# Performance work log

Hardware: AMD Instinct MI355X
Metric: run time of the kernel (lower is better)

Reference implementation:

```python
import jax, jax.numpy as jnp
import numpy as np

EPS = 1e-8

def _penalty(v, lo, hi):
    # if v<lo: (lo-v)/lo ; elif v>hi (hi finite): (v-hi)/hi ; else 0
    below = (lo - v) / lo
    if np.isinf(hi):
        return jnp.where(v < lo, below, 0.0)
    above = (v - hi) / hi
    return jnp.where(v < lo, below, jnp.where(v > hi, above, 0.0))

def _symbolic_features(x):
    # x: [B, input_dim]; column mapping from the original per-row loop
    am, bod, do, ph, nit = x[:, 0], x[:, 1], x[:, 2], x[:, 4], x[:, 7]
    # penalties in param_order = [ph, ammonia, bod, dissolved_oxygen, nitrate]
    p_ph  = _penalty(ph, 6.5, 8.5)
    p_am  = _penalty(am, 0.001, 0.5)
    p_bod = _penalty(bod, 0.001, 5.0)
    p_do  = _penalty(do, 6.0, np.inf)
    p_nit = _penalty(nit, 0.001, 10.0)
    # pollutant scores (missing params like 'nitrogen'/'orthophosphate' are skipped -> count adjusts)
    s_bact = (1.2 * am / (0.5 + EPS) + 1.5 * bod / (5.0 + EPS) - 0.8 * do / (10.0 + EPS)) / 3.0
    s_chem = (1.5 * ph / (8.5 + EPS) + 1.0 * nit / (10.0 + EPS)) / 2.0
    s_org  = (2.0 * bod / (5.0 + EPS) - 1.5 * do / (10.0 + EPS) + 0.8 * am / (0.5 + EPS)) / 3.0
    s_agr  = (2.0 * nit / (10.0 + EPS)) / 1.0
    resil = 1.0 / (1.0 + (p_ph + p_am + p_bod + p_do + p_nit) + EPS)
    return jnp.stack([p_ph, p_am, p_bod, p_do, p_nit, s_bact, s_chem, s_org, s_agr, resil], axis=1)

def setup_inputs() -> dict:
    key = jax.random.key(0)
    ks = jax.random.split(key, 16)
    B, D_IN, SYM, H = 1048576, 10, 10, 64
    def lin(k, fin, fout):
        k1, k2 = jax.random.split(k)
        s = 1.0 / np.sqrt(fin)
        return (jax.random.uniform(k1, (fin, fout), jnp.float32, -s, s),
                jax.random.uniform(k2, (fout,), jnp.float32, -s, s))
    W_sym, b_sym = lin(ks[0], SYM, H // 2)
    W_in, b_in = lin(ks[1], D_IN + H // 2, H)
    W1, b1 = lin(ks[2], H, H)
    W2, b2 = lin(ks[3], H, H)
    W3, b3 = lin(ks[4], H, H)
    W_r1, b_r1 = lin(ks[5], H, H // 2)
    W_r2, b_r2 = lin(ks[6], H // 2, 1)
    W_c1, b_c1 = lin(ks[7], H, H // 2)
    W_c2, b_c2 = lin(ks[8], H // 2, 4)
    x = jax.random.uniform(ks[9], (B, D_IN), jnp.float32)
    return {"x": x, "W_sym": W_sym, "b_sym": b_sym, "W_in": W_in, "b_in": b_in,
            "W1": W1, "b1": b1, "W2": W2, "b2": b2, "W3": W3, "b3": b3,
            "W_r1": W_r1, "b_r1": b_r1, "W_r2": W_r2, "b_r2": b_r2,
            "W_c1": W_c1, "b_c1": b_c1, "W_c2": W_c2, "b_c2": b_c2}

def reference(x, W_sym, b_sym, W_in, b_in, W1, b1, W2, b2, W3, b3,
              W_r1, b_r1, W_r2, b_r2, W_c1, b_c1, W_c2, b_c2):
    elu = jax.nn.elu
    sym = _symbolic_features(x)                      # [B, 10]
    sym_enc = elu(sym @ W_sym + b_sym)               # [B, 32]  (Dropout: eval mode = identity)
    h = elu(jnp.concatenate([x, sym_enc], axis=1) @ W_in + b_in)  # [B, 64]
    for W, b in ((W1, b1), (W2, b2), (W3, b3)):
        h = h + elu(h @ W + b)                       # residual MLP stack
    predictions = elu(h @ W_r1 + b_r1) @ W_r2 + b_r2            # [B, 1]
    pollutant_logits = elu(h @ W_c1 + b_c1) @ W_c2 + b_c2       # [B, 4]
    return predictions, pollutant_logits
```

## Files before the change

kernel.cpp:

```cpp
#include <hip/hip_runtime.h>
#include <hip/hip_bf16.h>
#include <math.h>

#define NROWS 1048576
#define EPSF 1e-8f

typedef unsigned short ushortT;
typedef __attribute__((ext_vector_type(8))) short short8;
typedef __attribute__((ext_vector_type(4))) float floatx4;
typedef __attribute__((ext_vector_type(4))) int intx4;

#define WS_HI   256
#define WS_LO   41216
#define WS_MF   82176
#define MF_B5   0
#define MF_WSYM 320
#define MF_BSYM 640
#define MF_WR2  672
#define MF_BR2  704
#define MF_WC2  708
#define MF_BC2  836
#define MF_WC2T 840

#define LDS_FENCE() asm volatile("s_waitcnt lgkmcnt(0)" ::: "memory")

struct WPtrs { const void* p[19]; };

__global__ void sniff_kernel(const ushortT* __restrict__ x, int* __restrict__ flag) {
    if (threadIdx.x == 0 && blockIdx.x == 0) {
        unsigned s = 0;
        for (int i = 0; i < 64; ++i) s |= (unsigned)(x[i] & 0x8000u);
        *flag = s ? 1 : 0;
    }
}

__device__ __forceinline__ float ldw(const void* p, int i, bool f32) {
    return f32 ? ((const float*)p)[i]
               : __uint_as_float(((unsigned)((const ushortT*)p)[i]) << 16);
}

__global__ void prep_kernel(WPtrs wp, const int* __restrict__ flag, void* __restrict__ ws) {
    const bool f32 = (*flag != 0);
    ushortT* hi = (ushortT*)((char*)ws + WS_HI);
    ushortT* lo = (ushortT*)((char*)ws + WS_LO);
    float* mf = (float*)((char*)ws + WS_MF);
    const int B = blockIdx.x;
    if (B < 5) {
        for (int idx = threadIdx.x; idx < 4096; idx += 256) {
            const int j = idx & 7, ln = (idx >> 3) & 63, t = (idx >> 9) & 3, s = idx >> 11;
            const int k = s * 32 + (ln >> 4) * 8 + j;
            const int n = t * 16 + (ln & 15);
            float w = 0.0f;
            if (B == 0)      { if (k < 42) w = ldw(wp.p[3], k * 64 + n, f32); }
            else if (B <= 3) { w = ldw(wp.p[3 + 2 * B], k * 64 + n, f32); }
            else             { w = (n < 32) ? ldw(wp.p[11], k * 32 + n, f32)
                                            : ldw(wp.p[15], k * 32 + (n - 32), f32); }
            const unsigned u = __float_as_uint(w);
            const float rem = w - __uint_as_float(u & 0xffff0000u);
            hi[B * 4096 + idx] = (ushortT)(u >> 16);
            lo[B * 4096 + idx] = (ushortT)(__float_as_uint(rem) >> 16);
        }
    } else {
        const int src[12] = {4, 6, 8, 10, 12, 16, 1, 2, 13, 14, 17, 18};
        const int cnt[12] = {64, 64, 64, 64, 32, 32, 320, 32, 32, 1, 128, 4};
        const int dst[12] = {0, 64, 128, 192, 256, 288, MF_WSYM, MF_BSYM, MF_WR2, MF_BR2, MF_WC2, MF_BC2};
        for (int a = 0; a < 12; ++a)
            for (int i = threadIdx.x; i < cnt[a]; i += 256)
                mf[dst[a] + i] = ldw(wp.p[src[a]], i, f32);
        for (int i = threadIdx.x; i < 128; i += 256) {
            const int qq = i >> 5, j = i & 31;
            mf[MF_WC2T + i] = ldw(wp.p[17], j * 4 + qq, f32);
        }
    }
}

__device__ __forceinline__ float eluf(float v) {
    return fmaxf(v, 0.0f) + (__expf(fminf(v, 0.0f)) - 1.0f);
}

__device__ __forceinline__ unsigned pack_hi16(unsigned ua, unsigned ub) {
    return __builtin_amdgcn_perm(ub, ua, 0x07060302u);
}

__device__ __forceinline__ void split8(const floatx4 f0, const floatx4 f1,
                                       short8& ahi, short8& alo) {
    float fv[8];
    #pragma unroll
    for (int i = 0; i < 4; ++i) { fv[i] = f0[i]; fv[4 + i] = f1[i]; }
    intx4 hi_i, lo_i;
    #pragma unroll
    for (int d = 0; d < 4; ++d) {
        const float a = fv[2 * d], b = fv[2 * d + 1];
        const unsigned ua = __float_as_uint(a), ub = __float_as_uint(b);
        hi_i[d] = (int)pack_hi16(ua, ub);
        const float la = a - __uint_as_float(ua & 0xffff0000u);
        const float lb = b - __uint_as_float(ub & 0xffff0000u);
        lo_i[d] = (int)pack_hi16(__float_as_uint(la), __float_as_uint(lb));
    }
    ahi = __builtin_bit_cast(short8, hi_i);
    alo = __builtin_bit_cast(short8, lo_i);
}

template<bool F32>
__device__ __forceinline__ void run_body(
    const void* __restrict__ xin, const char* __restrict__ wsb,
    void* __restrict__ out, float (* __restrict__ hb)[68],
    const int lane, const int rowg)
{
    const ushortT* __restrict__ wfhi = (const ushortT*)(wsb + WS_HI);
    const ushortT* __restrict__ wflo = (const ushortT*)(wsb + WS_LO);
    const float* __restrict__ mf = (const float*)(wsb + WS_MF);
    const int m = lane & 15, q = lane >> 4;

    #pragma unroll
    for (int it = 0; it < 6; ++it) {
        const int i = lane + (it << 6);
        if (i < 352) hb[i & 15][42 + (i >> 4)] = 0.0f;
    }

    float bias[5][4];
    #pragma unroll
    for (int L = 0; L < 5; ++L)
        #pragma unroll
        for (int t = 0; t < 4; ++t)
            bias[L][t] = mf[MF_B5 + L * 64 + t * 16 + m];

    float x[10];
    if (F32) {
        const float* xp = (const float*)xin + (size_t)rowg * 10;
        #pragma unroll
        for (int i = 0; i < 10; ++i) x[i] = xp[i];
    } else {
        const unsigned* xd = (const unsigned*)((const ushortT*)xin + (size_t)rowg * 10);
        #pragma unroll
        for (int i = 0; i < 5; ++i) {
            const unsigned d = xd[i];
            x[2 * i]     = __uint_as_float(d << 16);
            x[2 * i + 1] = __uint_as_float(d & 0xffff0000u);
        }
    }
    if (q == 0) {
        #pragma unroll
        for (int i = 0; i < 10; ++i) hb[m][i] = x[i];
    }

    const float am = x[0], bod = x[1], dox = x[2], ph = x[4], nit = x[7];
    const float p_ph  = ph  < 6.5f   ? (6.5f - ph) * 0.15384616f
                      : (ph > 8.5f   ? (ph - 8.5f) * 0.11764706f : 0.0f);
    const float p_am  = am  < 0.001f ? (0.001f - am) * 1000.0f
                      : (am > 0.5f   ? (am - 0.5f) * 2.0f : 0.0f);
    const float p_bod = bod < 0.001f ? (0.001f - bod) * 1000.0f
                      : (bod > 5.0f  ? (bod - 5.0f) * 0.2f : 0.0f);
    const float p_do  = dox < 6.0f   ? (6.0f - dox) * 0.16666667f : 0.0f;
    const float p_nit = nit < 0.001f ? (0.001f - nit) * 1000.0f
                      : (nit > 10.0f ? (nit - 10.0f) * 0.1f : 0.0f);
    const float s_bact = (am * 2.3999999f + bod * 0.29999998f - dox * 0.08f) * 0.33333334f;
    const float s_chem = (ph * 0.17647059f + nit * 0.1f) * 0.5f;
    const float s_org  = (bod * 0.39999998f - dox * 0.14999999f + am * 1.5999999f) * 0.33333334f;
    const float s_agr  = nit * 0.2f;
    const float resil  = 1.0f / (1.0f + (p_ph + p_am + p_bod + p_do + p_nit) + EPSF);
    const float sym[10] = {p_ph, p_am, p_bod, p_do, p_nit, s_bact, s_chem, s_org, s_agr, resil};

    float se[8];
    {
        const floatx4 b0 = *(const floatx4*)(mf + MF_BSYM + q * 8);
        const floatx4 b1 = *(const floatx4*)(mf + MF_BSYM + q * 8 + 4);
        #pragma unroll
        for (int jj = 0; jj < 4; ++jj) { se[jj] = b0[jj]; se[4 + jj] = b1[jj]; }
        #pragma unroll
        for (int k = 0; k < 10; ++k) {
            const floatx4 w0 = *(const floatx4*)(mf + MF_WSYM + k * 32 + q * 8);
            const floatx4 w1 = *(const floatx4*)(mf + MF_WSYM + k * 32 + q * 8 + 4);
            #pragma unroll
            for (int jj = 0; jj < 4; ++jj) {
                se[jj]     = fmaf(sym[k], w0[jj], se[jj]);
                se[4 + jj] = fmaf(sym[k], w1[jj], se[4 + jj]);
            }
        }
    }
    #pragma unroll
    for (int jj = 0; jj < 8; ++jj) hb[m][10 + q * 8 + jj] = eluf(se[jj]);
    LDS_FENCE();

    floatx4 hcd[4];
    #pragma unroll
    for (int L = 0; L < 5; ++L) {
        floatx4 acc[4];
        #pragma unroll
        for (int t = 0; t < 4; ++t) {
            const float b = bias[L][t];
            acc[t] = (floatx4){b, b, b, b};
        }
        #pragma unroll
        for (int s = 0; s < 2; ++s) {
            const floatx4 f0 = *(const floatx4*)&hb[m][s * 32 + q * 8];
            const floatx4 f1 = *(const floatx4*)&hb[m][s * 32 + q * 8 + 4];
            short8 ahi, alo;
            split8(f0, f1, ahi, alo);
            const int tbase = (L * 2 + s) << 2;
            #pragma unroll
            for (int t = 0; t < 4; ++t) {
                const short8 bh = *(const short8*)(wfhi + (size_t)((tbase + t) << 9) + lane * 8);
                acc[t] = __builtin_amdgcn_mfma_f32_16x16x32_bf16(ahi, bh, acc[t], 0, 0, 0);
                acc[t] = __builtin_amdgcn_mfma_f32_16x16x32_bf16(alo, bh, acc[t], 0, 0, 0);
                if (F32) {
                    const short8 bl = *(const short8*)(wflo + (size_t)((tbase + t) << 9) + lane * 8);
                    acc[t] = __builtin_amdgcn_mfma_f32_16x16x32_bf16(ahi, bl, acc[t], 0, 0, 0);
                }
            }
        }
        #pragma unroll
        for (int t = 0; t < 4; ++t) {
            #pragma unroll
            for (int r = 0; r < 4; ++r) {
                const float e = eluf(acc[t][r]);
                const float h = (L >= 1 && L <= 3) ? hcd[t][r] + e : e;
                hcd[t][r] = h;
                hb[(q << 2) + r][(t << 4) + m] = h;
            }
        }
        LDS_FENCE();
    }

    float accp = mf[MF_BR2];
    float accl = mf[MF_BC2 + q];
    const float* wct = mf + MF_WC2T + q * 32;
    #pragma unroll
    for (int jj = 0; jj < 8; ++jj) {
        const floatx4 hv = *(const floatx4*)&hb[m][jj * 4];
        const floatx4 hw = *(const floatx4*)&hb[m][32 + jj * 4];
        const floatx4 wc = *(const floatx4*)&wct[jj * 4];
        #pragma unroll
        for (int r = 0; r < 4; ++r) {
            accp = fmaf(hv[r], mf[MF_WR2 + jj * 4 + r], accp);
            accl = fmaf(hw[r], wc[r], accl);
        }
    }

    if (F32) {
        float* o = (float*)out;
        if (q == 0) o[rowg] = accp;
        o[NROWS + rowg * 4 + q] = accl;
    } else {
        __hip_bfloat16* o = (__hip_bfloat16*)out;
        if (q == 0) o[rowg] = __float2bfloat16(accp);
        o[NROWS + rowg * 4 + q] = __float2bfloat16(accl);
    }
}

__global__ __launch_bounds__(256, 4) void mlp_mfma_kernel(
    const void* __restrict__ xin, const int* __restrict__ flagp,
    const void* __restrict__ ws, void* __restrict__ out)
{
    __shared__ float hball[4][16][68];
    const int tid = threadIdx.x;
    const int wave = tid >> 6, lane = tid & 63;
    const int rowg = blockIdx.x * 64 + wave * 16 + (lane & 15);
    if (*flagp != 0)
        run_body<true>(xin, (const char*)ws, out, hball[wave], lane, rowg);
    else
        run_body<false>(xin, (const char*)ws, out, hball[wave], lane, rowg);
}

extern "C" void kernel_launch(void* const* d_in, const int* in_sizes, int n_in,
                              void* d_out, int out_size, void* d_ws, size_t ws_size,
                              hipStream_t stream) {
    (void)in_sizes; (void)n_in; (void)out_size; (void)ws_size;
    int* flag = (int*)d_ws;

    sniff_kernel<<<1, 64, 0, stream>>>((const ushortT*)d_in[0], flag);

    WPtrs wp;
    for (int i = 0; i < 19; ++i) wp.p[i] = d_in[i];
    prep_kernel<<<6, 256, 0, stream>>>(wp, flag, d_ws);

    mlp_mfma_kernel<<<NROWS / 64, 256, 0, stream>>>(d_in[0], flag, d_ws, d_out);
}
```

Before: 347.4 us.

## Keep activations in registers via transposed 16x16x16 MFMA chaining, drop LDS round-trips

The MLP is recast as W^T·h^T, with weights as the A operand and activations as the B operand, using 16x16x16 bf16 MFMAs. The accumulator layout of one layer then matches the B-operand layout of the next, so hidden states stay in registers between the five layers instead of being written to and reread from LDS after each layer. The head dot products are computed from registers and reduced across lanes with shuffles. The trade-off is twice as many smaller MFMA instructions and a re-tiled weight prep layout.

```diff
diff --git a/kernel.cpp b/kernel.cpp
--- a/kernel.cpp
+++ b/kernel.cpp
@@ -7,8 +7,9 @@
 
 typedef unsigned short ushortT;
 typedef __attribute__((ext_vector_type(8))) short short8;
+typedef __attribute__((ext_vector_type(4))) short short4v;
 typedef __attribute__((ext_vector_type(4))) float floatx4;
-typedef __attribute__((ext_vector_type(4))) int intx4;
+typedef __attribute__((ext_vector_type(2))) int int2v;
 
 #define WS_HI   256
 #define WS_LO   41216
@@ -46,19 +47,21 @@
     float* mf = (float*)((char*)ws + WS_MF);
     const int B = blockIdx.x;
     if (B < 5) {
+        const int L = B;
         for (int idx = threadIdx.x; idx < 4096; idx += 256) {
-            const int j = idx & 7, ln = (idx >> 3) & 63, t = (idx >> 9) & 3, s = idx >> 11;
-            const int k = s * 32 + (ln >> 4) * 8 + j;
-            const int n = t * 16 + (ln & 15);
+            const int j8 = idx & 7, ln = (idx >> 3) & 63, s2 = (idx >> 9) & 1, t = idx >> 10;
+            const int s = 2 * s2 + (j8 >> 2), j = j8 & 3;
+            const int k = 16 * s + 4 * (ln >> 4) + j;
+            const int m = 16 * t + (ln & 15);
             float w = 0.0f;
-            if (B == 0)      { if (k < 42) w = ldw(wp.p[3], k * 64 + n, f32); }
-            else if (B <= 3) { w = ldw(wp.p[3 + 2 * B], k * 64 + n, f32); }
-            else             { w = (n < 32) ? ldw(wp.p[11], k * 32 + n, f32)
-                                            : ldw(wp.p[15], k * 32 + (n - 32), f32); }
+            if (L == 0)      { if (k < 42) w = ldw(wp.p[3], k * 64 + m, f32); }
+            else if (L <= 3) { if (k < 64) w = ldw(wp.p[3 + 2 * L], k * 64 + m, f32); }
+            else             { if (k < 64) w = (m < 32) ? ldw(wp.p[11], k * 32 + m, f32)
+                                                        : ldw(wp.p[15], k * 32 + (m - 32), f32); }
             const unsigned u = __float_as_uint(w);
             const float rem = w - __uint_as_float(u & 0xffff0000u);
-            hi[B * 4096 + idx] = (ushortT)(u >> 16);
-            lo[B * 4096 + idx] = (ushortT)(__float_as_uint(rem) >> 16);
+            hi[L * 4096 + idx] = (ushortT)(u >> 16);
+            lo[L * 4096 + idx] = (ushortT)(__float_as_uint(rem) >> 16);
         }
     } else {
         const int src[12] = {4, 6, 8, 10, 12, 16, 1, 2, 13, 14, 17, 18};
@@ -82,23 +85,31 @@
     return __builtin_amdgcn_perm(ub, ua, 0x07060302u);
 }
 
-__device__ __forceinline__ void split8(const floatx4 f0, const floatx4 f1,
-                                       short8& ahi, short8& alo) {
-    float fv[8];
-    #pragma unroll
-    for (int i = 0; i < 4; ++i) { fv[i] = f0[i]; fv[4 + i] = f1[i]; }
-    intx4 hi_i, lo_i;
-    #pragma unroll
-    for (int d = 0; d < 4; ++d) {
-        const float a = fv[2 * d], b = fv[2 * d + 1];
-        const unsigned ua = __float_as_uint(a), ub = __float_as_uint(b);
-        hi_i[d] = (int)pack_hi16(ua, ub);
-        const float la = a - __uint_as_float(ua & 0xffff0000u);
-        const float lb = b - __uint_as_float(ub & 0xffff0000u);
-        lo_i[d] = (int)pack_hi16(__float_as_uint(la), __float_as_uint(lb));
-    }
-    ahi = __builtin_bit_cast(short8, hi_i);
-    alo = __builtin_bit_cast(short8, lo_i);
+__device__ __forceinline__ void split4(float a0, float a1, float a2, float a3,
+                                       short4v& h4, short4v& l4) {
+    const unsigned u0 = __float_as_uint(a0), u1 = __float_as_uint(a1);
+    const unsigned u2 = __float_as_uint(a2), u3 = __float_as_uint(a3);
+    int2v h, l;
+    h[0] = (int)pack_hi16(u0, u1);
+    h[1] = (int)pack_hi16(u2, u3);
+    const float l0 = a0 - __uint_as_float(u0 & 0xffff0000u);
+    const float l1 = a1 - __uint_as_float(u1 & 0xffff0000u);
+    const float l2 = a2 - __uint_as_float(u2 & 0xffff0000u);
+    const float l3 = a3 - __uint_as_float(u3 & 0xffff0000u);
+    l[0] = (int)pack_hi16(__float_as_uint(l0), __float_as_uint(l1));
+    l[1] = (int)pack_hi16(__float_as_uint(l2), __float_as_uint(l3));
+    h4 = __builtin_bit_cast(short4v, h);
+    l4 = __builtin_bit_cast(short4v, l);
+}
+
+__device__ __forceinline__ floatx4 mfma16(short4v a, short4v b, floatx4 c) {
+#if __has_builtin(__builtin_amdgcn_mfma_f32_16x16x16bf16_1k)
+    return __builtin_amdgcn_mfma_f32_16x16x16bf16_1k(a, b, c, 0, 0, 0);
+#else
+    floatx4 d;
+    asm("v_mfma_f32_16x16x16_bf16 %0, %1, %2, %3" : "=v"(d) : "v"(a), "v"(b), "v"(c));
+    return d;
+#endif
 }
 
 template<bool F32>
@@ -110,20 +121,7 @@
     const ushortT* __restrict__ wfhi = (const ushortT*)(wsb + WS_HI);
     const ushortT* __restrict__ wflo = (const ushortT*)(wsb + WS_LO);
     const float* __restrict__ mf = (const float*)(wsb + WS_MF);
-    const int m = lane & 15, q = lane >> 4;
-
-    #pragma unroll
-    for (int it = 0; it < 6; ++it) {
-        const int i = lane + (it << 6);
-        if (i < 352) hb[i & 15][42 + (i >> 4)] = 0.0f;
-    }
-
-    float bias[5][4];
-    #pragma unroll
-    for (int L = 0; L < 5; ++L)
-        #pragma unroll
-        for (int t = 0; t < 4; ++t)
-            bias[L][t] = mf[MF_B5 + L * 64 + t * 16 + m];
+    const int n = lane & 15, q = lane >> 4;
 
     float x[10];
     if (F32) {
@@ -141,7 +139,12 @@
     }
     if (q == 0) {
         #pragma unroll
-        for (int i = 0; i < 10; ++i) hb[m][i] = x[i];
+        for (int i = 0; i < 10; ++i) hb[n][i] = x[i];
+    }
+    #pragma unroll
+    for (int i = 0; i < 6; ++i) {
+        const int c = 42 + q * 6 + i;
+        if (c < 64) hb[n][c] = 0.0f;
     }
 
     const float am = x[0], bod = x[1], dox = x[2], ph = x[4], nit = x[7];
@@ -179,72 +182,99 @@
         }
     }
     #pragma unroll
-    for (int jj = 0; jj < 8; ++jj) hb[m][10 + q * 8 + jj] = eluf(se[jj]);
+    for (int jj = 0; jj < 8; ++jj) hb[n][10 + q * 8 + jj] = eluf(se[jj]);
     LDS_FENCE();
 
-    floatx4 hcd[4];
+    short4v Bhi[4], Blo[4];
+    #pragma unroll
+    for (int s = 0; s < 4; ++s) {
+        const floatx4 v = *(const floatx4*)&hb[n][16 * s + 4 * q];
+        split4(v[0], v[1], v[2], v[3], Bhi[s], Blo[s]);
+    }
+
+    float hprev[4][4];
+    float z[4][4];
     #pragma unroll
     for (int L = 0; L < 5; ++L) {
         floatx4 acc[4];
         #pragma unroll
-        for (int t = 0; t < 4; ++t) {
-            const float b = bias[L][t];
-            acc[t] = (floatx4){b, b, b, b};
-        }
-        #pragma unroll
-        for (int s = 0; s < 2; ++s) {
-            const floatx4 f0 = *(const floatx4*)&hb[m][s * 32 + q * 8];
-            const floatx4 f1 = *(const floatx4*)&hb[m][s * 32 + q * 8 + 4];
-            short8 ahi, alo;
-            split8(f0, f1, ahi, alo);
-            const int tbase = (L * 2 + s) << 2;
+        for (int t = 0; t < 4; ++t)
+            acc[t] = *(const floatx4*)(mf + MF_B5 + L * 64 + 16 * t + 4 * q);
+        #pragma unroll
+        for (int s2 = 0; s2 < 2; ++s2) {
             #pragma unroll
             for (int t = 0; t < 4; ++t) {
-                const short8 bh = *(const short8*)(wfhi + (size_t)((tbase + t) << 9) + lane * 8);
-                acc[t] = __builtin_amdgcn_mfma_f32_16x16x32_bf16(ahi, bh, acc[t], 0, 0, 0);
-                acc[t] = __builtin_amdgcn_mfma_f32_16x16x32_bf16(alo, bh, acc[t], 0, 0, 0);
+                const int off = L * 4096 + (t * 2 + s2) * 512 + lane * 8;
+                const short8 Ap = *(const short8*)(wfhi + off);
+                const short4v ae = {Ap[0], Ap[1], Ap[2], Ap[3]};
+                const short4v ao = {Ap[4], Ap[5], Ap[6], Ap[7]};
+                acc[t] = mfma16(ae, Bhi[2 * s2],     acc[t]);
+                acc[t] = mfma16(ae, Blo[2 * s2],     acc[t]);
+                acc[t] = mfma16(ao, Bhi[2 * s2 + 1], acc[t]);
+                acc[t] = mfma16(ao, Blo[2 * s2 + 1], acc[t]);
                 if (F32) {
-                    const short8 bl = *(const short8*)(wflo + (size_t)((tbase + t) << 9) + lane * 8);
-                    acc[t] = __builtin_amdgcn_mfma_f32_16x16x32_bf16(ahi, bl, acc[t], 0, 0, 0);
+                    const short8 Alp = *(const short8*)(wflo + off);
+                    const short4v le = {Alp[0], Alp[1], Alp[2], Alp[3]};
+                    const short4v lo_ = {Alp[4], Alp[5], Alp[6], Alp[7]};
+                    acc[t] = mfma16(le,  Bhi[2 * s2],     acc[t]);
+                    acc[t] = mfma16(lo_, Bhi[2 * s2 + 1], acc[t]);
                 }
             }
         }
-        #pragma unroll
-        for (int t = 0; t < 4; ++t) {
-            #pragma unroll
-            for (int r = 0; r < 4; ++r) {
-                const float e = eluf(acc[t][r]);
-                const float h = (L >= 1 && L <= 3) ? hcd[t][r] + e : e;
-                hcd[t][r] = h;
-                hb[(q << 2) + r][(t << 4) + m] = h;
+        if (L < 4) {
+            #pragma unroll
+            for (int t = 0; t < 4; ++t) {
+                #pragma unroll
+                for (int r = 0; r < 4; ++r) {
+                    const float e = eluf(acc[t][r]);
+                    hprev[t][r] = (L >= 1) ? hprev[t][r] + e : e;
+                }
+                split4(hprev[t][0], hprev[t][1], hprev[t][2], hprev[t][3], Bhi[t], Blo[t]);
             }
-        }
-        LDS_FENCE();
-    }
-
-    float accp = mf[MF_BR2];
-    float accl = mf[MF_BC2 + q];
-    const float* wct = mf + MF_WC2T + q * 32;
-    #pragma unroll
-    for (int jj = 0; jj < 8; ++jj) {
-        const floatx4 hv = *(const floatx4*)&hb[m][jj * 4];
-        const floatx4 hw = *(const floatx4*)&hb[m][32 + jj * 4];
-        const floatx4 wc = *(const floatx4*)&wct[jj * 4];
-        #pragma unroll
-        for (int r = 0; r < 4; ++r) {
-            accp = fmaf(hv[r], mf[MF_WR2 + jj * 4 + r], accp);
-            accl = fmaf(hw[r], wc[r], accl);
-        }
-    }
+        } else {
+            #pragma unroll
+            for (int t = 0; t < 4; ++t)
+                #pragma unroll
+                for (int r = 0; r < 4; ++r)
+                    z[t][r] = eluf(acc[t][r]);
+        }
+    }
+
+    float pred = (q == 0) ? mf[MF_BR2] : 0.0f;
+    #pragma unroll
+    for (int t = 0; t < 2; ++t) {
+        const floatx4 w = *(const floatx4*)(mf + MF_WR2 + 16 * t + 4 * q);
+        #pragma unroll
+        for (int r = 0; r < 4; ++r) pred = fmaf(z[t][r], w[r], pred);
+    }
+    float lg[4];
+    #pragma unroll
+    for (int c = 0; c < 4; ++c) {
+        lg[c] = (q == 0) ? mf[MF_BC2 + c] : 0.0f;
+        #pragma unroll
+        for (int t = 0; t < 2; ++t) {
+            const floatx4 w = *(const floatx4*)(mf + MF_WC2T + c * 32 + 16 * t + 4 * q);
+            #pragma unroll
+            for (int r = 0; r < 4; ++r) lg[c] = fmaf(z[2 + t][r], w[r], lg[c]);
+        }
+    }
+    pred += __shfl_xor(pred, 16, 64);
+    pred += __shfl_xor(pred, 32, 64);
+    #pragma unroll
+    for (int c = 0; c < 4; ++c) {
+        lg[c] += __shfl_xor(lg[c], 16, 64);
+        lg[c] += __shfl_xor(lg[c], 32, 64);
+    }
+    const float lsel = q == 0 ? lg[0] : (q == 1 ? lg[1] : (q == 2 ? lg[2] : lg[3]));
 
     if (F32) {
         float* o = (float*)out;
-        if (q == 0) o[rowg] = accp;
-        o[NROWS + rowg * 4 + q] = accl;
+        if (q == 0) o[rowg] = pred;
+        o[NROWS + rowg * 4 + q] = lsel;
     } else {
         __hip_bfloat16* o = (__hip_bfloat16*)out;
-        if (q == 0) o[rowg] = __float2bfloat16(accp);
-        o[NROWS + rowg * 4 + q] = __float2bfloat16(accl);
+        if (q == 0) o[rowg] = __float2bfloat16(pred);
+        o[NROWS + rowg * 4 + q] = __float2bfloat16(lsel);
     }
 }
 
```

After: 367.4 us. 1.06x slower.
